# Kernel optimization log

Measured on AMD Instinct MI355X. Metric: run time of the kernel, lower is better.

## Reference

```python
import jax, jax.numpy as jnp
import numpy as np

ASSIGN_RATIO = 0.1  # hard-coded inside coarsen_graph in the original
EPS_CUT = 1e-7
EPS_NORM = 1e-12  # torch F.normalize eps


def _normalize_batch_adj(adj):
    # adj: [B, N, N]
    n = adj.shape[1]
    A = adj + jnp.eye(n, dtype=adj.dtype)
    deg_inv_sqrt = jnp.clip(A.sum(-1), 1.0, None) ** -0.5  # [B, N]
    newA = deg_inv_sqrt[..., :, None] * A * deg_inv_sqrt[..., None, :]
    row_mask = (adj.sum(-1) > 0).astype(adj.dtype)  # [B, N]
    return row_mask[..., :, None] * newA


def setup_inputs():
    key = jax.random.key(0)
    k0, k1, k2, k3, k4 = jax.random.split(key, 5)
    B, N, D, T = 512, 128, 256, 512
    concept_hidden = jax.random.normal(k0, (B, N, D), jnp.float32)
    adj = jax.random.uniform(k1, (B, N, N), jnp.float32)
    head = jax.random.randint(k2, (B, T), 0, N)
    lin_w = jax.random.normal(k3, (1, D), jnp.float32) / np.sqrt(D).astype(np.float32)
    bias = jax.random.normal(k4, (1,), jnp.float32)
    return {"concept_hidden": concept_hidden, "adj": adj, "head": head,
            "lin_w": lin_w, "bias": bias}


def reference(concept_hidden, adj, head, lin_w, bias):
    # concept_hidden: [B, N, D], adj: [B, N, N], head: [B, T] node indices
    x = concept_hidden
    B, N, D = x.shape

    out = x @ lin_w.T                      # [B, N, 1]  self.lin(x)
    norm_adj = _normalize_batch_adj(adj)   # [B, N, N]
    out = norm_adj @ out + bias            # [B, N, 1]
    alpha = jax.nn.sigmoid(out ** 2)[..., 0]  # [B, N]

    # batch_num_nodes[i] = len(set(head[i]))  -> count unique via sort
    hs = jnp.sort(head, axis=-1)
    n_uniq = 1 + (hs[:, 1:] != hs[:, :-1]).sum(-1)  # [B]

    # per-sample k = ceil(n * 0.1) + 1 (only when n > 1); cut = k-th largest alpha
    k = jnp.ceil(n_uniq.astype(jnp.float32) * ASSIGN_RATIO).astype(jnp.int32) + 1
    a_desc = jnp.sort(alpha, axis=-1)[:, ::-1]       # descending
    idx = jnp.clip(k - 1, 0, N - 1)
    cut = jnp.take_along_axis(a_desc, idx[:, None], axis=-1)[:, 0]
    cut = jnp.where(n_uniq > 1, cut, jnp.zeros_like(cut))  # [B]

    cut_alpha = jax.nn.relu(alpha + EPS_CUT - cut[:, None])  # [B, N]

    # S = norm_adj * cut_alpha broadcast over rows, then L1-normalize rows
    S = norm_adj * cut_alpha[:, None, :]
    S = S / jnp.clip(jnp.abs(S).sum(-1, keepdims=True), EPS_NORM, None)

    St = jnp.swapaxes(S, 1, 2)             # [B, N, N]
    embedding_tensor = St @ x              # S^T x   [B, N, D]
    new_adj = (St @ adj) @ S               # S^T A S [B, N, N]
    return embedding_tensor, new_adj
```

## Files before the change

kernel.cpp:

```cpp
#include <hip/hip_runtime.h>

#define Bsz 512
#define Nn  128
#define Dd  256
#define Tt  512

typedef __attribute__((ext_vector_type(8))) short short8;
typedef __attribute__((ext_vector_type(4))) float f32x4;

__device__ __forceinline__ ushort f2bf(float f) {
    union { float f; unsigned u; } v; v.f = f;
    unsigned r = v.u + 0x7fffu + ((v.u >> 16) & 1u);
    return (ushort)(r >> 16);
}
__device__ __forceinline__ unsigned pk2(float a, float b) {
    return (unsigned)f2bf(a) | ((unsigned)f2bf(b) << 16);
}
__device__ __forceinline__ short8 pk8(const float* v) {
    union { uint4 u; short8 s; } c;
    c.u.x = pk2(v[0], v[1]); c.u.y = pk2(v[2], v[3]);
    c.u.z = pk2(v[4], v[5]); c.u.w = pk2(v[6], v[7]);
    return c.s;
}

__global__ __launch_bounds__(256) void mega(
    const float* __restrict__ x, const float* __restrict__ adj,
    const int* __restrict__ head, const float* __restrict__ lin_w,
    const float* __restrict__ bias,
    float* __restrict__ emb, float* __restrict__ nadj)
{
    const int b = blockIdx.x, t = threadIdx.x;
    __shared__ __align__(16) float bufA[Nn][132];
    __shared__ __align__(16) ushort STl[Nn][136];
    __shared__ float wS[Dd];
    __shared__ float ttS[Nn], disS[Nn], maskS[Nn], alphaS[Nn], uS[Nn], rowcS[Nn];
    __shared__ float partS[Nn][2];
    __shared__ float dotP[Nn][2];
    __shared__ int   flags[Nn];
    __shared__ int   nuniq;
    __shared__ float cutS;

    const float bias0 = bias[0];
    wS[t] = lin_w[t];
    if (t < Nn) flags[t] = 0;
    if (t == 0) { nuniq = 0; cutS = 0.f; }

    const float* adjb = adj + (size_t)b * Nn * Nn;
#pragma unroll
    for (int i = 0; i < 16; ++i) {
        int f = t + 256 * i;
        int rr = f >> 5, c = (f & 31) * 4;
        *(float4*)&bufA[rr][c] = *(const float4*)&adjb[(size_t)rr * Nn + c];
    }
    __syncthreads();

    { int h0 = head[(size_t)b * Tt + t];
      int h1 = head[(size_t)b * Tt + 256 + t];
      flags[h0] = 1; flags[h1] = 1; }

    {
        const int dr = t >> 1, dh = t & 1;
        const float4* xr = (const float4*)(x + ((size_t)b * Nn + dr) * Dd + dh * 128);
        float p = 0.f;
#pragma unroll 8
        for (int i = 0; i < 32; ++i) {
            float4 v = xr[i];
            const float* w = &wS[dh * 128 + 4 * i];
            p += v.x * w[0] + v.y * w[1] + v.z * w[2] + v.w * w[3];
        }
        dotP[dr][dh] = p;
    }

    const int r = t >> 1, hh = t & 1, cb = hh * 64;
    {
        float4 s4 = {0.f, 0.f, 0.f, 0.f};
#pragma unroll
        for (int j = 0; j < 16; ++j) {
            float4 v = *(float4*)&bufA[r][cb + 4 * j];
            s4.x += v.x; s4.y += v.y; s4.z += v.z; s4.w += v.w;
        }
        partS[r][hh] = (s4.x + s4.y) + (s4.z + s4.w);
    }
    __syncthreads();

    if (t < Nn) {
        float rs  = partS[t][0] + partS[t][1];
        maskS[t]  = (rs > 0.f) ? 1.f : 0.f;
        float dis = 1.f / sqrtf(fmaxf(rs + 1.f, 1.f));
        disS[t]   = dis;
        ttS[t]    = dis * (dotP[t][0] + dotP[t][1]);
        atomicAdd(&nuniq, flags[t]);
    }
    __syncthreads();

    {
        float4 a = {0.f, 0.f, 0.f, 0.f};
#pragma unroll
        for (int j = 0; j < 16; ++j) {
            float4 v = *(float4*)&bufA[r][cb + 4 * j];
            float4 w = *(float4*)&ttS[cb + 4 * j];
            a.x += v.x * w.x; a.y += v.y * w.y; a.z += v.z * w.z; a.w += v.w * w.w;
        }
        partS[r][hh] = (a.x + a.y) + (a.z + a.w);
    }
    __syncthreads();
    if (t < Nn) {
        float mv = partS[t][0] + partS[t][1];
        float o  = maskS[t] * disS[t] * (mv + ttS[t]) + bias0;
        alphaS[t] = 1.f / (1.f + expf(-o * o));
    }
    __syncthreads();
    if (t < Nn) {
        int nu = nuniq;
        if (nu > 1) {
            int idx = (int)ceilf((float)nu * 0.1f);
            if (idx > Nn - 1) idx = Nn - 1;
            float an = alphaS[t];
            int cg = 0, ce = 0;
            for (int j = 0; j < Nn; ++j) {
                float aj = alphaS[j];
                cg += (aj > an); ce += (aj == an);
            }
            if (cg <= idx && idx < cg + ce) cutS = an;
        }
    }
    __syncthreads();
    if (t < Nn) uS[t] = fmaxf(alphaS[t] + 1e-7f - cutS, 0.f) * disS[t];
    __syncthreads();
    {
        float4 a = {0.f, 0.f, 0.f, 0.f};
#pragma unroll
        for (int j = 0; j < 16; ++j) {
            float4 v = *(float4*)&bufA[r][cb + 4 * j];
            float4 w = *(float4*)&uS[cb + 4 * j];
            a.x += v.x * w.x; a.y += v.y * w.y; a.z += v.z * w.z; a.w += v.w * w.w;
        }
        partS[r][hh] = (a.x + a.y) + (a.z + a.w);
    }
    __syncthreads();
    if (t < Nn) {
        float tot  = partS[t][0] + partS[t][1] + uS[t];
        float rsum = maskS[t] * disS[t] * tot;
        rowcS[t]   = maskS[t] * disS[t] / fmaxf(rsum, 1e-12f);
    }
    __syncthreads();

    {
        const int m = r;
        const float um = uS[m];
#pragma unroll
        for (int kc = 0; kc < 8; ++kc) {
            int k0 = cb + kc * 8;
            float vv[8];
#pragma unroll
            for (int j = 0; j < 8; ++j) {
                int k = k0 + j;
                vv[j] = rowcS[k] * (bufA[k][m] + ((k == m) ? 1.f : 0.f)) * um;
            }
            uint4 pkv;
            pkv.x = pk2(vv[0], vv[1]); pkv.y = pk2(vv[2], vv[3]);
            pkv.z = pk2(vv[4], vv[5]); pkv.w = pk2(vv[6], vv[7]);
            *(uint4*)&STl[m][k0] = pkv;
        }
    }
    __syncthreads();

    const int lane = t & 63, wv = t >> 6;
    const int l15 = lane & 15, quad = lane >> 4;
    const int m0 = wv * 32;
    f32x4 acc[2][8];
#pragma unroll
    for (int mt = 0; mt < 2; ++mt)
#pragma unroll
        for (int nt = 0; nt < 8; ++nt) acc[mt][nt] = (f32x4){0.f, 0.f, 0.f, 0.f};

#pragma unroll
    for (int k0 = 0; k0 < 128; k0 += 32) {
        float av[8];
        *(float4*)&av[0] = *(float4*)&bufA[m0 + l15][k0 + quad * 8];
        *(float4*)&av[4] = *(float4*)&bufA[m0 + l15][k0 + quad * 8 + 4];
        short8 a0 = pk8(av);
        *(float4*)&av[0] = *(float4*)&bufA[m0 + 16 + l15][k0 + quad * 8];
        *(float4*)&av[4] = *(float4*)&bufA[m0 + 16 + l15][k0 + quad * 8 + 4];
        short8 a1 = pk8(av);
        short8 bf[8];
#pragma unroll
        for (int nt = 0; nt < 8; ++nt)
            bf[nt] = *(const short8*)&STl[nt * 16 + l15][k0 + quad * 8];
#pragma unroll
        for (int nt = 0; nt < 8; ++nt) {
            acc[0][nt] = __builtin_amdgcn_mfma_f32_16x16x32_bf16(a0, bf[nt], acc[0][nt], 0, 0, 0);
            acc[1][nt] = __builtin_amdgcn_mfma_f32_16x16x32_bf16(a1, bf[nt], acc[1][nt], 0, 0, 0);
        }
    }
    __syncthreads();

    ushort (*PT)[136] = (ushort(*)[136])&bufA[0][0];
#pragma unroll
    for (int mt = 0; mt < 2; ++mt)
#pragma unroll
        for (int nt = 0; nt < 8; ++nt) {
            int j    = nt * 16 + l15;
            int mcol = m0 + mt * 16 + quad * 4;
            uint2 w;
            w.x = pk2(acc[mt][nt][0], acc[mt][nt][1]);
            w.y = pk2(acc[mt][nt][2], acc[mt][nt][3]);
            *(uint2*)&PT[j][mcol] = w;
        }
    __syncthreads();

#pragma unroll
    for (int mt = 0; mt < 2; ++mt)
#pragma unroll
        for (int nt = 0; nt < 8; ++nt) acc[mt][nt] = (f32x4){0.f, 0.f, 0.f, 0.f};

#pragma unroll
    for (int k0 = 0; k0 < 128; k0 += 32) {
        short8 a0 = *(const short8*)&STl[m0 + l15][k0 + quad * 8];
        short8 a1 = *(const short8*)&STl[m0 + 16 + l15][k0 + quad * 8];
        short8 bf[8];
#pragma unroll
        for (int nt = 0; nt < 8; ++nt)
            bf[nt] = *(const short8*)&PT[nt * 16 + l15][k0 + quad * 8];
#pragma unroll
        for (int nt = 0; nt < 8; ++nt) {
            acc[0][nt] = __builtin_amdgcn_mfma_f32_16x16x32_bf16(a0, bf[nt], acc[0][nt], 0, 0, 0);
            acc[1][nt] = __builtin_amdgcn_mfma_f32_16x16x32_bf16(a1, bf[nt], acc[1][nt], 0, 0, 0);
        }
    }
#pragma unroll
    for (int mt = 0; mt < 2; ++mt)
#pragma unroll
        for (int nt = 0; nt < 8; ++nt)
#pragma unroll
            for (int rr = 0; rr < 4; ++rr) {
                int row = m0 + mt * 16 + quad * 4 + rr;
                int col = nt * 16 + l15;
                nadj[((size_t)b * Nn + row) * Nn + col] = acc[mt][nt][rr];
            }
    __syncthreads();

    float (*xbufF)[132] = (float(*)[132])&bufA[0][0];
    short8 aE[2][4];
#pragma unroll
    for (int ks = 0; ks < 4; ++ks) {
        aE[0][ks] = *(const short8*)&STl[m0 + l15][ks * 32 + quad * 8];
        aE[1][ks] = *(const short8*)&STl[m0 + 16 + l15][ks * 32 + quad * 8];
    }
    for (int qd = 0; qd < 4; ++qd) {
        const int d0 = qd * 64;
#pragma unroll
        for (int i = 0; i < 8; ++i) {
            int f = t + 256 * i;
            int k = f >> 4, c4 = (f & 15) * 4;
            float4 v = *(const float4*)&x[((size_t)b * Nn + k) * Dd + d0 + c4];
            xbufF[c4    ][k] = v.x; xbufF[c4 + 1][k] = v.y;
            xbufF[c4 + 2][k] = v.z; xbufF[c4 + 3][k] = v.w;
        }
        __syncthreads();
        f32x4 accE[2][4];
#pragma unroll
        for (int mt = 0; mt < 2; ++mt)
#pragma unroll
            for (int nt = 0; nt < 4; ++nt) accE[mt][nt] = (f32x4){0.f, 0.f, 0.f, 0.f};
#pragma unroll
        for (int ks = 0; ks < 4; ++ks) {
            short8 bf[4];
#pragma unroll
            for (int nt = 0; nt < 4; ++nt) {
                float bv[8];
                *(float4*)&bv[0] = *(float4*)&xbufF[nt * 16 + l15][ks * 32 + quad * 8];
                *(float4*)&bv[4] = *(float4*)&xbufF[nt * 16 + l15][ks * 32 + quad * 8 + 4];
                bf[nt] = pk8(bv);
            }
#pragma unroll
            for (int nt = 0; nt < 4; ++nt) {
                accE[0][nt] = __builtin_amdgcn_mfma_f32_16x16x32_bf16(aE[0][ks], bf[nt], accE[0][nt], 0, 0, 0);
                accE[1][nt] = __builtin_amdgcn_mfma_f32_16x16x32_bf16(aE[1][ks], bf[nt], accE[1][nt], 0, 0, 0);
            }
        }
#pragma unroll
        for (int mt = 0; mt < 2; ++mt)
#pragma unroll
            for (int nt = 0; nt < 4; ++nt)
#pragma unroll
                for (int rr = 0; rr < 4; ++rr) {
                    int row = m0 + mt * 16 + quad * 4 + rr;
                    int col = d0 + nt * 16 + l15;
                    emb[((size_t)b * Nn + row) * Dd + col] = accE[mt][nt][rr];
                }
        __syncthreads();
    }
}

extern "C" void kernel_launch(void* const* d_in, const int* in_sizes, int n_in,
                              void* d_out, int out_size, void* d_ws, size_t ws_size,
                              hipStream_t stream)
{
    const float* x     = (const float*)d_in[0];
    const float* adj   = (const float*)d_in[1];
    const int*   head  = (const int*)d_in[2];
    const float* lin_w = (const float*)d_in[3];
    const float* bias  = (const float*)d_in[4];

    float* emb  = (float*)d_out;
    float* nadj = emb + (size_t)Bsz * Nn * Dd;

    mega<<<Bsz, 256, 0, stream>>>(x, adj, head, lin_w, bias, emb, nadj);
}
```

Before: 217.4 us.

## Expand fused per-graph kernel from 256 to 1024 threads with redistributed work

Each block now runs 1024 threads instead of 256. Every phase is re-partitioned across them: row reductions use 8 segments per row, the two MFMA GEMMs give each of 16 waves one 16-row tile and half the columns, and the embedding GEMM splits the D columns across wave halves. The x staging buffer is also re-laid out from a transposed [d][k] array to a [k][65] array. The aim is more parallelism and latency hiding per graph, since 512 blocks of 4 waves underfill the GPU. In exchange there is more per-wave overhead, A-fragment loads are duplicated across waves, the new x buffer is read with scalar strided accesses, and register limits are tighter under the 1024-thread bound.

```diff
diff --git a/kernel.cpp b/kernel.cpp
--- a/kernel.cpp
+++ b/kernel.cpp
@@ -23,7 +23,7 @@
     return c.s;
 }
 
-__global__ __launch_bounds__(256) void mega(
+__global__ __launch_bounds__(1024) void mega(
     const float* __restrict__ x, const float* __restrict__ adj,
     const int* __restrict__ head, const float* __restrict__ lin_w,
     const float* __restrict__ bias,
@@ -34,61 +34,61 @@
     __shared__ __align__(16) ushort STl[Nn][136];
     __shared__ float wS[Dd];
     __shared__ float ttS[Nn], disS[Nn], maskS[Nn], alphaS[Nn], uS[Nn], rowcS[Nn];
-    __shared__ float partS[Nn][2];
-    __shared__ float dotP[Nn][2];
+    __shared__ float partS[Nn][9];
+    __shared__ float dotP[Nn][9];
     __shared__ int   flags[Nn];
     __shared__ int   nuniq;
     __shared__ float cutS;
 
     const float bias0 = bias[0];
-    wS[t] = lin_w[t];
+    if (t < Dd) wS[t] = lin_w[t];
     if (t < Nn) flags[t] = 0;
     if (t == 0) { nuniq = 0; cutS = 0.f; }
 
     const float* adjb = adj + (size_t)b * Nn * Nn;
 #pragma unroll
-    for (int i = 0; i < 16; ++i) {
-        int f = t + 256 * i;
+    for (int i = 0; i < 4; ++i) {
+        int f = t + 1024 * i;
         int rr = f >> 5, c = (f & 31) * 4;
         *(float4*)&bufA[rr][c] = *(const float4*)&adjb[(size_t)rr * Nn + c];
     }
     __syncthreads();
 
-    { int h0 = head[(size_t)b * Tt + t];
-      int h1 = head[(size_t)b * Tt + 256 + t];
-      flags[h0] = 1; flags[h1] = 1; }
-
-    {
-        const int dr = t >> 1, dh = t & 1;
-        const float4* xr = (const float4*)(x + ((size_t)b * Nn + dr) * Dd + dh * 128);
+    if (t < Tt) { int h = head[(size_t)b * Tt + t]; flags[h] = 1; }
+
+    {
+        const int dr = t >> 3, dh = t & 7;
+        const float4* xr = (const float4*)(x + ((size_t)b * Nn + dr) * Dd + dh * 32);
         float p = 0.f;
-#pragma unroll 8
-        for (int i = 0; i < 32; ++i) {
+#pragma unroll
+        for (int i = 0; i < 8; ++i) {
             float4 v = xr[i];
-            const float* w = &wS[dh * 128 + 4 * i];
+            const float* w = &wS[dh * 32 + 4 * i];
             p += v.x * w[0] + v.y * w[1] + v.z * w[2] + v.w * w[3];
         }
         dotP[dr][dh] = p;
     }
 
-    const int r = t >> 1, hh = t & 1, cb = hh * 64;
+    const int r = t >> 3, seg = t & 7, cbs = seg * 16;
     {
         float4 s4 = {0.f, 0.f, 0.f, 0.f};
 #pragma unroll
-        for (int j = 0; j < 16; ++j) {
-            float4 v = *(float4*)&bufA[r][cb + 4 * j];
+        for (int j = 0; j < 4; ++j) {
+            float4 v = *(float4*)&bufA[r][cbs + 4 * j];
             s4.x += v.x; s4.y += v.y; s4.z += v.z; s4.w += v.w;
         }
-        partS[r][hh] = (s4.x + s4.y) + (s4.z + s4.w);
-    }
-    __syncthreads();
-
-    if (t < Nn) {
-        float rs  = partS[t][0] + partS[t][1];
+        partS[r][seg] = (s4.x + s4.y) + (s4.z + s4.w);
+    }
+    __syncthreads();
+
+    if (t < Nn) {
+        float rs = 0.f, dt = 0.f;
+#pragma unroll
+        for (int j = 0; j < 8; ++j) { rs += partS[t][j]; dt += dotP[t][j]; }
         maskS[t]  = (rs > 0.f) ? 1.f : 0.f;
         float dis = 1.f / sqrtf(fmaxf(rs + 1.f, 1.f));
         disS[t]   = dis;
-        ttS[t]    = dis * (dotP[t][0] + dotP[t][1]);
+        ttS[t]    = dis * dt;
         atomicAdd(&nuniq, flags[t]);
     }
     __syncthreads();
@@ -96,17 +96,19 @@
     {
         float4 a = {0.f, 0.f, 0.f, 0.f};
 #pragma unroll
-        for (int j = 0; j < 16; ++j) {
-            float4 v = *(float4*)&bufA[r][cb + 4 * j];
-            float4 w = *(float4*)&ttS[cb + 4 * j];
+        for (int j = 0; j < 4; ++j) {
+            float4 v = *(float4*)&bufA[r][cbs + 4 * j];
+            float4 w = *(float4*)&ttS[cbs + 4 * j];
             a.x += v.x * w.x; a.y += v.y * w.y; a.z += v.z * w.z; a.w += v.w * w.w;
         }
-        partS[r][hh] = (a.x + a.y) + (a.z + a.w);
-    }
-    __syncthreads();
-    if (t < Nn) {
-        float mv = partS[t][0] + partS[t][1];
-        float o  = maskS[t] * disS[t] * (mv + ttS[t]) + bias0;
+        partS[r][seg] = (a.x + a.y) + (a.z + a.w);
+    }
+    __syncthreads();
+    if (t < Nn) {
+        float mv = 0.f;
+#pragma unroll
+        for (int j = 0; j < 8; ++j) mv += partS[t][j];
+        float o = maskS[t] * disS[t] * (mv + ttS[t]) + bias0;
         alphaS[t] = 1.f / (1.f + expf(-o * o));
     }
     __syncthreads();
@@ -130,165 +132,139 @@
     {
         float4 a = {0.f, 0.f, 0.f, 0.f};
 #pragma unroll
-        for (int j = 0; j < 16; ++j) {
-            float4 v = *(float4*)&bufA[r][cb + 4 * j];
-            float4 w = *(float4*)&uS[cb + 4 * j];
+        for (int j = 0; j < 4; ++j) {
+            float4 v = *(float4*)&bufA[r][cbs + 4 * j];
+            float4 w = *(float4*)&uS[cbs + 4 * j];
             a.x += v.x * w.x; a.y += v.y * w.y; a.z += v.z * w.z; a.w += v.w * w.w;
         }
-        partS[r][hh] = (a.x + a.y) + (a.z + a.w);
-    }
-    __syncthreads();
-    if (t < Nn) {
-        float tot  = partS[t][0] + partS[t][1] + uS[t];
+        partS[r][seg] = (a.x + a.y) + (a.z + a.w);
+    }
+    __syncthreads();
+    if (t < Nn) {
+        float tot = uS[t];
+#pragma unroll
+        for (int j = 0; j < 8; ++j) tot += partS[t][j];
         float rsum = maskS[t] * disS[t] * tot;
         rowcS[t]   = maskS[t] * disS[t] / fmaxf(rsum, 1e-12f);
     }
     __syncthreads();
 
     {
-        const int m = r;
+        const int m = t & 127, sl = t >> 7, k0 = sl * 16;
         const float um = uS[m];
-#pragma unroll
-        for (int kc = 0; kc < 8; ++kc) {
-            int k0 = cb + kc * 8;
-            float vv[8];
-#pragma unroll
-            for (int j = 0; j < 8; ++j) {
-                int k = k0 + j;
-                vv[j] = rowcS[k] * (bufA[k][m] + ((k == m) ? 1.f : 0.f)) * um;
-            }
-            uint4 pkv;
-            pkv.x = pk2(vv[0], vv[1]); pkv.y = pk2(vv[2], vv[3]);
-            pkv.z = pk2(vv[4], vv[5]); pkv.w = pk2(vv[6], vv[7]);
-            *(uint4*)&STl[m][k0] = pkv;
-        }
-    }
-    __syncthreads();
-
-    const int lane = t & 63, wv = t >> 6;
+        float vv[16];
+#pragma unroll
+        for (int j = 0; j < 16; ++j) {
+            int k = k0 + j;
+            vv[j] = rowcS[k] * (bufA[k][m] + ((k == m) ? 1.f : 0.f)) * um;
+        }
+        uint4 p0, p1;
+        p0.x = pk2(vv[0],  vv[1]);  p0.y = pk2(vv[2],  vv[3]);
+        p0.z = pk2(vv[4],  vv[5]);  p0.w = pk2(vv[6],  vv[7]);
+        p1.x = pk2(vv[8],  vv[9]);  p1.y = pk2(vv[10], vv[11]);
+        p1.z = pk2(vv[12], vv[13]); p1.w = pk2(vv[14], vv[15]);
+        *(uint4*)&STl[m][k0]     = p0;
+        *(uint4*)&STl[m][k0 + 8] = p1;
+    }
+    __syncthreads();
+
+    const int lane = t & 63, w = t >> 6;
     const int l15 = lane & 15, quad = lane >> 4;
-    const int m0 = wv * 32;
-    f32x4 acc[2][8];
-#pragma unroll
-    for (int mt = 0; mt < 2; ++mt)
-#pragma unroll
-        for (int nt = 0; nt < 8; ++nt) acc[mt][nt] = (f32x4){0.f, 0.f, 0.f, 0.f};
-
+    const int mrow  = (w & 7) * 16;
+    const int nhalf = (w >> 3) * 64;
+    f32x4 acc[4];
+
+#pragma unroll
+    for (int nt = 0; nt < 4; ++nt) acc[nt] = (f32x4){0.f, 0.f, 0.f, 0.f};
 #pragma unroll
     for (int k0 = 0; k0 < 128; k0 += 32) {
         float av[8];
-        *(float4*)&av[0] = *(float4*)&bufA[m0 + l15][k0 + quad * 8];
-        *(float4*)&av[4] = *(float4*)&bufA[m0 + l15][k0 + quad * 8 + 4];
+        *(float4*)&av[0] = *(float4*)&bufA[mrow + l15][k0 + quad * 8];
+        *(float4*)&av[4] = *(float4*)&bufA[mrow + l15][k0 + quad * 8 + 4];
         short8 a0 = pk8(av);
-        *(float4*)&av[0] = *(float4*)&bufA[m0 + 16 + l15][k0 + quad * 8];
-        *(float4*)&av[4] = *(float4*)&bufA[m0 + 16 + l15][k0 + quad * 8 + 4];
-        short8 a1 = pk8(av);
-        short8 bf[8];
-#pragma unroll
-        for (int nt = 0; nt < 8; ++nt)
-            bf[nt] = *(const short8*)&STl[nt * 16 + l15][k0 + quad * 8];
-#pragma unroll
-        for (int nt = 0; nt < 8; ++nt) {
-            acc[0][nt] = __builtin_amdgcn_mfma_f32_16x16x32_bf16(a0, bf[nt], acc[0][nt], 0, 0, 0);
-            acc[1][nt] = __builtin_amdgcn_mfma_f32_16x16x32_bf16(a1, bf[nt], acc[1][nt], 0, 0, 0);
+#pragma unroll
+        for (int nt = 0; nt < 4; ++nt) {
+            short8 bf = *(const short8*)&STl[nhalf + nt * 16 + l15][k0 + quad * 8];
+            acc[nt] = __builtin_amdgcn_mfma_f32_16x16x32_bf16(a0, bf, acc[nt], 0, 0, 0);
         }
     }
     __syncthreads();
 
     ushort (*PT)[136] = (ushort(*)[136])&bufA[0][0];
 #pragma unroll
-    for (int mt = 0; mt < 2; ++mt)
-#pragma unroll
-        for (int nt = 0; nt < 8; ++nt) {
-            int j    = nt * 16 + l15;
-            int mcol = m0 + mt * 16 + quad * 4;
-            uint2 w;
-            w.x = pk2(acc[mt][nt][0], acc[mt][nt][1]);
-            w.y = pk2(acc[mt][nt][2], acc[mt][nt][3]);
-            *(uint2*)&PT[j][mcol] = w;
-        }
-    __syncthreads();
-
-#pragma unroll
-    for (int mt = 0; mt < 2; ++mt)
-#pragma unroll
-        for (int nt = 0; nt < 8; ++nt) acc[mt][nt] = (f32x4){0.f, 0.f, 0.f, 0.f};
-
+    for (int nt = 0; nt < 4; ++nt) {
+        int j    = nhalf + nt * 16 + l15;
+        int mcol = mrow + quad * 4;
+        uint2 wv2;
+        wv2.x = pk2(acc[nt][0], acc[nt][1]);
+        wv2.y = pk2(acc[nt][2], acc[nt][3]);
+        *(uint2*)&PT[j][mcol] = wv2;
+    }
+    __syncthreads();
+
+#pragma unroll
+    for (int nt = 0; nt < 4; ++nt) acc[nt] = (f32x4){0.f, 0.f, 0.f, 0.f};
 #pragma unroll
     for (int k0 = 0; k0 < 128; k0 += 32) {
-        short8 a0 = *(const short8*)&STl[m0 + l15][k0 + quad * 8];
-        short8 a1 = *(const short8*)&STl[m0 + 16 + l15][k0 + quad * 8];
-        short8 bf[8];
-#pragma unroll
-        for (int nt = 0; nt < 8; ++nt)
-            bf[nt] = *(const short8*)&PT[nt * 16 + l15][k0 + quad * 8];
-#pragma unroll
-        for (int nt = 0; nt < 8; ++nt) {
-            acc[0][nt] = __builtin_amdgcn_mfma_f32_16x16x32_bf16(a0, bf[nt], acc[0][nt], 0, 0, 0);
-            acc[1][nt] = __builtin_amdgcn_mfma_f32_16x16x32_bf16(a1, bf[nt], acc[1][nt], 0, 0, 0);
-        }
-    }
-#pragma unroll
-    for (int mt = 0; mt < 2; ++mt)
-#pragma unroll
-        for (int nt = 0; nt < 8; ++nt)
-#pragma unroll
-            for (int rr = 0; rr < 4; ++rr) {
-                int row = m0 + mt * 16 + quad * 4 + rr;
-                int col = nt * 16 + l15;
-                nadj[((size_t)b * Nn + row) * Nn + col] = acc[mt][nt][rr];
-            }
-    __syncthreads();
-
-    float (*xbufF)[132] = (float(*)[132])&bufA[0][0];
-    short8 aE[2][4];
-#pragma unroll
-    for (int ks = 0; ks < 4; ++ks) {
-        aE[0][ks] = *(const short8*)&STl[m0 + l15][ks * 32 + quad * 8];
-        aE[1][ks] = *(const short8*)&STl[m0 + 16 + l15][ks * 32 + quad * 8];
-    }
+        short8 a0 = *(const short8*)&STl[mrow + l15][k0 + quad * 8];
+#pragma unroll
+        for (int nt = 0; nt < 4; ++nt) {
+            short8 bf = *(const short8*)&PT[nhalf + nt * 16 + l15][k0 + quad * 8];
+            acc[nt] = __builtin_amdgcn_mfma_f32_16x16x32_bf16(a0, bf, acc[nt], 0, 0, 0);
+        }
+    }
+#pragma unroll
+    for (int nt = 0; nt < 4; ++nt)
+#pragma unroll
+        for (int rr = 0; rr < 4; ++rr) {
+            int row = mrow + quad * 4 + rr;
+            int col = nhalf + nt * 16 + l15;
+            nadj[((size_t)b * Nn + row) * Nn + col] = acc[nt][rr];
+        }
+    __syncthreads();
+
+    float (*xbufK)[65] = (float(*)[65])&bufA[0][0];
+    short8 aE[4];
+#pragma unroll
+    for (int ks = 0; ks < 4; ++ks)
+        aE[ks] = *(const short8*)&STl[mrow + l15][ks * 32 + quad * 8];
+    const int dcb = (w >> 3) * 32;
+
     for (int qd = 0; qd < 4; ++qd) {
         const int d0 = qd * 64;
 #pragma unroll
-        for (int i = 0; i < 8; ++i) {
-            int f = t + 256 * i;
+        for (int i = 0; i < 2; ++i) {
+            int f = t + 1024 * i;
             int k = f >> 4, c4 = (f & 15) * 4;
             float4 v = *(const float4*)&x[((size_t)b * Nn + k) * Dd + d0 + c4];
-            xbufF[c4    ][k] = v.x; xbufF[c4 + 1][k] = v.y;
-            xbufF[c4 + 2][k] = v.z; xbufF[c4 + 3][k] = v.w;
+            xbufK[k][c4]     = v.x; xbufK[k][c4 + 1] = v.y;
+            xbufK[k][c4 + 2] = v.z; xbufK[k][c4 + 3] = v.w;
         }
         __syncthreads();
-        f32x4 accE[2][4];
-#pragma unroll
-        for (int mt = 0; mt < 2; ++mt)
-#pragma unroll
-            for (int nt = 0; nt < 4; ++nt) accE[mt][nt] = (f32x4){0.f, 0.f, 0.f, 0.f};
+        f32x4 accE[2];
+        accE[0] = (f32x4){0.f, 0.f, 0.f, 0.f};
+        accE[1] = (f32x4){0.f, 0.f, 0.f, 0.f};
 #pragma unroll
         for (int ks = 0; ks < 4; ++ks) {
-            short8 bf[4];
-#pragma unroll
-            for (int nt = 0; nt < 4; ++nt) {
+#pragma unroll
+            for (int s = 0; s < 2; ++s) {
+                const int dcol = dcb + s * 16;
                 float bv[8];
-                *(float4*)&bv[0] = *(float4*)&xbufF[nt * 16 + l15][ks * 32 + quad * 8];
-                *(float4*)&bv[4] = *(float4*)&xbufF[nt * 16 + l15][ks * 32 + quad * 8 + 4];
-                bf[nt] = pk8(bv);
+#pragma unroll
+                for (int j = 0; j < 8; ++j)
+                    bv[j] = xbufK[ks * 32 + quad * 8 + j][dcol + l15];
+                short8 bf = pk8(bv);
+                accE[s] = __builtin_amdgcn_mfma_f32_16x16x32_bf16(aE[ks], bf, accE[s], 0, 0, 0);
             }
-#pragma unroll
-            for (int nt = 0; nt < 4; ++nt) {
-                accE[0][nt] = __builtin_amdgcn_mfma_f32_16x16x32_bf16(aE[0][ks], bf[nt], accE[0][nt], 0, 0, 0);
-                accE[1][nt] = __builtin_amdgcn_mfma_f32_16x16x32_bf16(aE[1][ks], bf[nt], accE[1][nt], 0, 0, 0);
+        }
+#pragma unroll
+        for (int s = 0; s < 2; ++s)
+#pragma unroll
+            for (int rr = 0; rr < 4; ++rr) {
+                int row = mrow + quad * 4 + rr;
+                int col = d0 + dcb + s * 16 + l15;
+                emb[((size_t)b * Nn + row) * Dd + col] = accE[s][rr];
             }
-        }
-#pragma unroll
-        for (int mt = 0; mt < 2; ++mt)
-#pragma unroll
-            for (int nt = 0; nt < 4; ++nt)
-#pragma unroll
-                for (int rr = 0; rr < 4; ++rr) {
-                    int row = m0 + mt * 16 + quad * 4 + rr;
-                    int col = d0 + nt * 16 + l15;
-                    emb[((size_t)b * Nn + row) * Dd + col] = accE[mt][nt][rr];
-                }
         __syncthreads();
     }
 }
@@ -306,5 +282,5 @@
     float* emb  = (float*)d_out;
     float* nadj = emb + (size_t)Bsz * Nn * Dd;
 
-    mega<<<Bsz, 256, 0, stream>>>(x, adj, head, lin_w, bias, emb, nadj);
-}
+    mega<<<Bsz, 1024, 0, stream>>>(x, adj, head, lin_w, bias, emb, nadj);
+}
```

Result: no change. 214.4 us (-1.4%).
